# Kernel optimization log

Measured on AMD Instinct MI355X. Metric: run time of the kernel, lower is better.

Reference implementation:

```python
import jax, jax.numpy as jnp
import numpy as np

T, N, D = 4096, 128, 128
NEG = -1.0e9


def setup_inputs() -> dict:
    key = jax.random.key(0)
    k1, k2, k3, k4 = jax.random.split(key, 4)
    return {
        "query": jax.random.normal(k1, (N, D), dtype=jnp.float32),
        "key": jax.random.normal(k2, (T, N, D), dtype=jnp.float32),
        "value": jax.random.normal(k3, (T, N, D), dtype=jnp.float32),
        "lens_for_attention": jax.random.randint(k4, (N,), 1, T + 1, dtype=jnp.int64 if jax.config.jax_enable_x64 else jnp.int32),
    }


def reference(query, key, value, lens_for_attention):
    # key, value: (T, N, D) -> (N, T, D)
    k = jnp.transpose(key, (1, 0, 2))
    v = jnp.transpose(value, (1, 0, 2))
    t = k.shape[1]
    # mask: True where timestep index >= length (padded positions)
    mask = jnp.arange(t)[None, :] >= lens_for_attention[:, None]  # (N, T)
    # energy = bmm(key, query): (N, T, D) @ (N, D) -> (N, T)
    energy = jnp.einsum('ntd,nd->nt', k, query)
    energy = jnp.where(mask, NEG, energy)
    attention = jax.nn.softmax(energy, axis=1)  # (N, T)
    # context = bmm(attention, value): (N, T) @ (N, T, D) -> (N, D)
    out = jnp.einsum('nt,ntd->nd', attention, v)
    return (out, attention)
```

## Files before the change

kernel.cpp:

```cpp
#include <hip/hip_runtime.h>

#define T_DIM 4096
#define N_DIM 128
#define D_DIM 128
#define CHUNK 256
#define NCHUNK (T_DIM / CHUNK)
#define NEGE (-1.0e9f)

__global__ __launch_bounds__(256) void energy_kernel(
    const float* __restrict__ q,
    const float* __restrict__ key,
    const int*   __restrict__ lens,
    float*       __restrict__ att,
    float*       __restrict__ blockmax)
{
    const int b    = blockIdx.x;
    const int n    = b & (N_DIM - 1);
    const int c    = b >> 7;
    const int t0   = c * CHUNK;
    const int len  = lens[n];
    const int tid  = threadIdx.x;

    if (t0 >= len) {
        att[(size_t)n * T_DIM + t0 + tid] = NEGE;
        if (tid == 0) blockmax[n * NCHUNK + c] = NEGE;
        return;
    }

    const int wave = tid >> 6;
    const int lane = tid & 63;
    const int half = lane >> 5;
    const int l32  = lane & 31;

    const float4 qv = *(const float4*)(q + n * D_DIM + l32 * 4);

    float lmax = NEGE;

    #pragma unroll 4
    for (int i = 0; i < CHUNK / 8; ++i) {
        const int t = t0 + wave * 2 + i * 8 + half;
        float e;
        if (t < len) {
            const float4 kv = *(const float4*)(key + (size_t)t * (N_DIM * D_DIM)
                                               + n * D_DIM + l32 * 4);
            float p = kv.x * qv.x + kv.y * qv.y + kv.z * qv.z + kv.w * qv.w;
            p += __shfl_xor(p, 1);
            p += __shfl_xor(p, 2);
            p += __shfl_xor(p, 4);
            p += __shfl_xor(p, 8);
            p += __shfl_xor(p, 16);
            e = p;
        } else {
            e = NEGE;
        }
        if (l32 == 0) att[(size_t)n * T_DIM + t] = e;
        lmax = fmaxf(lmax, e);
    }

    lmax = fmaxf(lmax, __shfl_xor(lmax, 32));
    __shared__ float smax[4];
    if (lane == 0) smax[wave] = lmax;
    __syncthreads();
    if (tid == 0) {
        blockmax[n * NCHUNK + c] =
            fmaxf(fmaxf(smax[0], smax[1]), fmaxf(smax[2], smax[3]));
    }
}

__global__ __launch_bounds__(256) void softmax_kernel(
    float* __restrict__ att,
    const float* __restrict__ blockmax,
    float* __restrict__ out)
{
    const int n   = blockIdx.x;
    const int tid = threadIdx.x;
    const int wave = tid >> 6;
    const int lane = tid & 63;

    __shared__ float smaxarr[NCHUNK];
    __shared__ float ssum[4];
    __shared__ float stot;

    if (tid < NCHUNK) smaxarr[tid] = blockmax[n * NCHUNK + tid];
    if (tid < 32) ((float4*)(out + n * D_DIM))[tid] = make_float4(0.f, 0.f, 0.f, 0.f);
    __syncthreads();
    float m = smaxarr[0];
    #pragma unroll
    for (int i = 1; i < NCHUNK; ++i) m = fmaxf(m, smaxarr[i]);

    float4* row = (float4*)(att + (size_t)n * T_DIM);
    float4 vals[4];
    float sum = 0.f;
    #pragma unroll
    for (int i = 0; i < 4; ++i) {
        float4 v = row[tid + i * 256];
        v.x = __expf(v.x - m);
        v.y = __expf(v.y - m);
        v.z = __expf(v.z - m);
        v.w = __expf(v.w - m);
        sum += v.x + v.y + v.z + v.w;
        vals[i] = v;
    }
    sum += __shfl_xor(sum, 1);
    sum += __shfl_xor(sum, 2);
    sum += __shfl_xor(sum, 4);
    sum += __shfl_xor(sum, 8);
    sum += __shfl_xor(sum, 16);
    sum += __shfl_xor(sum, 32);
    if (lane == 0) ssum[wave] = sum;
    __syncthreads();
    if (tid == 0) stot = ssum[0] + ssum[1] + ssum[2] + ssum[3];
    __syncthreads();
    const float inv = 1.0f / stot;

    #pragma unroll
    for (int i = 0; i < 4; ++i) {
        float4 v = vals[i];
        v.x *= inv; v.y *= inv; v.z *= inv; v.w *= inv;
        row[tid + i * 256] = v;
    }
}

__global__ __launch_bounds__(256) void pv_kernel(
    const float* __restrict__ att,
    const float* __restrict__ value,
    const int*   __restrict__ lens,
    float*       __restrict__ out)
{
    const int b    = blockIdx.x;
    const int n    = b & (N_DIM - 1);
    const int c    = b >> 7;
    const int t0   = c * CHUNK;
    const int len  = lens[n];

    if (t0 >= len) return;

    const int tid  = threadIdx.x;
    const int qd   = tid & 31;
    const int g    = tid >> 5;
    const int tend = min(t0 + CHUNK, len);

    float4 acc = make_float4(0.f, 0.f, 0.f, 0.f);
    #pragma unroll 4
    for (int t = t0 + g; t < tend; t += 8) {
        const float a = att[(size_t)n * T_DIM + t];
        const float4 v = *(const float4*)(value + (size_t)t * (N_DIM * D_DIM)
                                          + n * D_DIM + qd * 4);
        acc.x += a * v.x;
        acc.y += a * v.y;
        acc.z += a * v.z;
        acc.w += a * v.w;
    }

    __shared__ float4 buf[256];
    buf[tid] = acc;
    __syncthreads();
    if (tid < 128) {
        float4 o = buf[tid + 128];
        buf[tid].x += o.x; buf[tid].y += o.y; buf[tid].z += o.z; buf[tid].w += o.w;
    }
    __syncthreads();
    if (tid < 64) {
        float4 o = buf[tid + 64];
        buf[tid].x += o.x; buf[tid].y += o.y; buf[tid].z += o.z; buf[tid].w += o.w;
    }
    __syncthreads();
    if (tid < 32) {
        float4 a0 = buf[tid];
        float4 a1 = buf[tid + 32];
        float* dst = out + n * D_DIM + tid * 4;
        atomicAdd(dst + 0, a0.x + a1.x);
        atomicAdd(dst + 1, a0.y + a1.y);
        atomicAdd(dst + 2, a0.z + a1.z);
        atomicAdd(dst + 3, a0.w + a1.w);
    }
}

extern "C" void kernel_launch(void* const* d_in, const int* in_sizes, int n_in,
                              void* d_out, int out_size, void* d_ws, size_t ws_size,
                              hipStream_t stream) {
    const float* q     = (const float*)d_in[0];
    const float* key   = (const float*)d_in[1];
    const float* value = (const float*)d_in[2];
    const int*   lens  = (const int*)d_in[3];

    float* out = (float*)d_out;
    float* att = out + N_DIM * D_DIM;

    float* blockmax = (float*)d_ws;

    energy_kernel <<<N_DIM * NCHUNK, 256, 0, stream>>>(q, key, lens, att, blockmax);
    softmax_kernel<<<N_DIM,          256, 0, stream>>>(att, blockmax, out);
    pv_kernel     <<<N_DIM * NCHUNK, 256, 0, stream>>>(att, value, lens, out);
}
```

Before: 479.9 us.

## Fold softmax into energy and PV kernels using per-chunk max/sum combination

Removes the standalone softmax kernel. The energy kernel now also computes a per-chunk sum of exponentials relative to the chunk max. The PV kernel merges all chunk max/sum pairs online to get the global normaliser, normalises its own chunk of the attention row in place, and reads the probabilities from shared memory. This drops one launch and a full extra read/write pass over the attention matrix, at the cost of every PV block redoing the small 16-entry combine and using more registers in the energy kernel.

```diff
diff --git a/kernel.cpp b/kernel.cpp
--- a/kernel.cpp
+++ b/kernel.cpp
@@ -12,7 +12,9 @@
     const float* __restrict__ key,
     const int*   __restrict__ lens,
     float*       __restrict__ att,
-    float*       __restrict__ blockmax)
+    float*       __restrict__ blockmax,
+    float*       __restrict__ blocksum,
+    float*       __restrict__ out)
 {
     const int b    = blockIdx.x;
     const int n    = b & (N_DIM - 1);
@@ -22,10 +24,18 @@
     const int tid  = threadIdx.x;
 
     if (t0 >= len) {
-        att[(size_t)n * T_DIM + t0 + tid] = NEGE;
-        if (tid == 0) blockmax[n * NCHUNK + c] = NEGE;
+        if (tid < 64)
+            ((float4*)(att + (size_t)n * T_DIM + t0))[tid] =
+                make_float4(NEGE, NEGE, NEGE, NEGE);
+        if (tid == 0) {
+            blockmax[n * NCHUNK + c] = NEGE;
+            blocksum[n * NCHUNK + c] = 0.0f;
+        }
         return;
     }
+
+    if (c == 0 && tid < 32)
+        ((float4*)(out + n * D_DIM))[tid] = make_float4(0.f, 0.f, 0.f, 0.f);
 
     const int wave = tid >> 6;
     const int lane = tid & 63;
@@ -34,9 +44,10 @@
 
     const float4 qv = *(const float4*)(q + n * D_DIM + l32 * 4);
 
+    float evals[CHUNK / 8];
     float lmax = NEGE;
 
-    #pragma unroll 4
+    #pragma unroll
     for (int i = 0; i < CHUNK / 8; ++i) {
         const int t = t0 + wave * 2 + i * 8 + half;
         float e;
@@ -54,77 +65,35 @@
             e = NEGE;
         }
         if (l32 == 0) att[(size_t)n * T_DIM + t] = e;
+        evals[i] = e;
         lmax = fmaxf(lmax, e);
     }
 
     lmax = fmaxf(lmax, __shfl_xor(lmax, 32));
     __shared__ float smax[4];
+    __shared__ float ssum[4];
     if (lane == 0) smax[wave] = lmax;
     __syncthreads();
+    const float m = fmaxf(fmaxf(smax[0], smax[1]), fmaxf(smax[2], smax[3]));
+
+    float s = 0.f;
+    #pragma unroll
+    for (int i = 0; i < CHUNK / 8; ++i) s += __expf(evals[i] - m);
+    s += __shfl_xor(s, 32);
+    if (lane == 0) ssum[wave] = s;
+    __syncthreads();
     if (tid == 0) {
-        blockmax[n * NCHUNK + c] =
-            fmaxf(fmaxf(smax[0], smax[1]), fmaxf(smax[2], smax[3]));
+        blockmax[n * NCHUNK + c] = m;
+        blocksum[n * NCHUNK + c] = ssum[0] + ssum[1] + ssum[2] + ssum[3];
     }
 }
 
-__global__ __launch_bounds__(256) void softmax_kernel(
-    float* __restrict__ att,
-    const float* __restrict__ blockmax,
-    float* __restrict__ out)
-{
-    const int n   = blockIdx.x;
-    const int tid = threadIdx.x;
-    const int wave = tid >> 6;
-    const int lane = tid & 63;
-
-    __shared__ float smaxarr[NCHUNK];
-    __shared__ float ssum[4];
-    __shared__ float stot;
-
-    if (tid < NCHUNK) smaxarr[tid] = blockmax[n * NCHUNK + tid];
-    if (tid < 32) ((float4*)(out + n * D_DIM))[tid] = make_float4(0.f, 0.f, 0.f, 0.f);
-    __syncthreads();
-    float m = smaxarr[0];
-    #pragma unroll
-    for (int i = 1; i < NCHUNK; ++i) m = fmaxf(m, smaxarr[i]);
-
-    float4* row = (float4*)(att + (size_t)n * T_DIM);
-    float4 vals[4];
-    float sum = 0.f;
-    #pragma unroll
-    for (int i = 0; i < 4; ++i) {
-        float4 v = row[tid + i * 256];
-        v.x = __expf(v.x - m);
-        v.y = __expf(v.y - m);
-        v.z = __expf(v.z - m);
-        v.w = __expf(v.w - m);
-        sum += v.x + v.y + v.z + v.w;
-        vals[i] = v;
-    }
-    sum += __shfl_xor(sum, 1);
-    sum += __shfl_xor(sum, 2);
-    sum += __shfl_xor(sum, 4);
-    sum += __shfl_xor(sum, 8);
-    sum += __shfl_xor(sum, 16);
-    sum += __shfl_xor(sum, 32);
-    if (lane == 0) ssum[wave] = sum;
-    __syncthreads();
-    if (tid == 0) stot = ssum[0] + ssum[1] + ssum[2] + ssum[3];
-    __syncthreads();
-    const float inv = 1.0f / stot;
-
-    #pragma unroll
-    for (int i = 0; i < 4; ++i) {
-        float4 v = vals[i];
-        v.x *= inv; v.y *= inv; v.z *= inv; v.w *= inv;
-        row[tid + i * 256] = v;
-    }
-}
-
 __global__ __launch_bounds__(256) void pv_kernel(
-    const float* __restrict__ att,
+    float*       __restrict__ att,
     const float* __restrict__ value,
     const int*   __restrict__ lens,
+    const float* __restrict__ blockmax,
+    const float* __restrict__ blocksum,
     float*       __restrict__ out)
 {
     const int b    = blockIdx.x;
@@ -132,10 +101,44 @@
     const int c    = b >> 7;
     const int t0   = c * CHUNK;
     const int len  = lens[n];
-
-    if (t0 >= len) return;
-
     const int tid  = threadIdx.x;
+
+    if (t0 >= len) {
+        if (tid < 64)
+            ((float4*)(att + (size_t)n * T_DIM + t0))[tid] =
+                make_float4(0.f, 0.f, 0.f, 0.f);
+        return;
+    }
+
+    __shared__ float sm[NCHUNK], ss[NCHUNK];
+    __shared__ float sp[CHUNK];
+    if (tid < NCHUNK) {
+        sm[tid] = blockmax[n * NCHUNK + tid];
+        ss[tid] = blocksum[n * NCHUNK + tid];
+    }
+    __syncthreads();
+
+    float m = sm[0];
+    #pragma unroll
+    for (int i = 1; i < NCHUNK; ++i) m = fmaxf(m, sm[i]);
+    float Z = 0.f;
+    #pragma unroll
+    for (int i = 0; i < NCHUNK; ++i) Z += ss[i] * __expf(sm[i] - m);
+    const float inv = 1.0f / Z;
+
+    if (tid < 64) {
+        float4* arow = (float4*)(att + (size_t)n * T_DIM + t0);
+        float4 e4 = arow[tid];
+        float4 p4;
+        p4.x = __expf(e4.x - m) * inv;
+        p4.y = __expf(e4.y - m) * inv;
+        p4.z = __expf(e4.z - m) * inv;
+        p4.w = __expf(e4.w - m) * inv;
+        arow[tid] = p4;
+        ((float4*)sp)[tid] = p4;
+    }
+    __syncthreads();
+
     const int qd   = tid & 31;
     const int g    = tid >> 5;
     const int tend = min(t0 + CHUNK, len);
@@ -143,7 +146,7 @@
     float4 acc = make_float4(0.f, 0.f, 0.f, 0.f);
     #pragma unroll 4
     for (int t = t0 + g; t < tend; t += 8) {
-        const float a = att[(size_t)n * T_DIM + t];
+        const float a = sp[t - t0];
         const float4 v = *(const float4*)(value + (size_t)t * (N_DIM * D_DIM)
                                           + n * D_DIM + qd * 4);
         acc.x += a * v.x;
@@ -188,8 +191,10 @@
     float* att = out + N_DIM * D_DIM;
 
     float* blockmax = (float*)d_ws;
-
-    energy_kernel <<<N_DIM * NCHUNK, 256, 0, stream>>>(q, key, lens, att, blockmax);
-    softmax_kernel<<<N_DIM,          256, 0, stream>>>(att, blockmax, out);
-    pv_kernel     <<<N_DIM * NCHUNK, 256, 0, stream>>>(att, value, lens, out);
+    float* blocksum = (float*)((char*)d_ws + 8192);
+
+    energy_kernel<<<N_DIM * NCHUNK, 256, 0, stream>>>(q, key, lens, att,
+                                                      blockmax, blocksum, out);
+    pv_kernel    <<<N_DIM * NCHUNK, 256, 0, stream>>>(att, value, lens,
+                                                      blockmax, blocksum, out);
 }
```

After: 477.1 us. No clear change (-0.6%).
